# Kernel optimization log

Measured on AMD Instinct MI355X. Metric: run time of the kernel, lower is better.

The kernel has to match this reference:

```python
import jax, jax.numpy as jnp
import numpy as np

IN_CH, OUT_CH, HID, NHEAD = 4, 1, 256, 8
VDIM = HID // NHEAD
LOCALITIES = (2.0, 10.0, 10.0, 10.0, 10.0, 200.0)
N_BLOCKS = len(LOCALITIES) - 2
INPUT_RES, LATENT_RES, OUTPUT_RES = (64, 64), (32, 32), (64, 64)
BATCH = 8


def pairwise_dist(res1x, res1y, res2x, res2y):
    gx1 = jnp.linspace(0, 1, res1x + 1)[:-1]
    gy1 = jnp.linspace(0, 1, res1y + 1)[:-1]
    g1x, g1y = jnp.meshgrid(gx1, gy1, indexing='xy')
    grid1 = jnp.stack([g1x.flatten(), g1y.flatten()], axis=-1)
    gx2 = jnp.linspace(0, 1, res2x + 1)[:-1]
    gy2 = jnp.linspace(0, 1, res2y + 1)[:-1]
    g2x, g2y = jnp.meshgrid(gx2, gy2, indexing='xy')
    grid2 = jnp.stack([g2x.flatten(), g2y.flatten()], axis=-1)
    diff = grid1[:, None, :] - grid2[None, :, :]
    return (jnp.sum(diff ** 2, axis=-1) / 2.0).astype(jnp.float32)


def pos_att(m_dist, x, r, w, locality):
    # m_dist:[Nq,Nk]  x:[B,Nk,HID]  r:[H,1,1]  w:[H,HID,VDIM]
    scale = jnp.tan(0.25 * jnp.pi * (1 - 1e-07) * (1 + jnp.sin(r)))
    sd = m_dist[None, :, :] * scale  # [H,Nq,Nk]
    if locality <= 100:
        thr = jnp.percentile(sd, locality, axis=-1, keepdims=True)
        sd = jnp.where(sd <= thr, sd, jnp.inf)
    att = jax.nn.softmax(-sd, axis=-1)  # [H,Nq,Nk]
    value = jnp.einsum('bnj,hjk->bhnk', x, w)  # [B,H,Nk,VDIM]
    out = jnp.einsum('hjn,bhnk->bhjk', att, value)  # [B,H,Nq,VDIM]
    out = jnp.transpose(out, (0, 2, 1, 3)).reshape(x.shape[0], m_dist.shape[0], -1)
    return jax.nn.gelu(out)


def lin(x, w, b):
    # eqx.nn.Linear: w:[out,in], b:[out]
    return jnp.einsum('bni,oi->bno', x, w) + b


def setup_inputs() -> dict:
    key = jax.random.key(0)
    ks = jax.random.split(key, 20)
    Ni = INPUT_RES[0] * INPUT_RES[1]
    s_h = 1.0 / jnp.sqrt(HID)
    s_in = 1.0 / jnp.sqrt(IN_CH)
    return {
        'x': jax.random.normal(ks[0], (BATCH, Ni, IN_CH), jnp.float32),
        'en_fc1_w': jax.random.uniform(ks[1], (HID, IN_CH), jnp.float32, -s_in, s_in),
        'en_fc1_b': jax.random.uniform(ks[2], (HID,), jnp.float32, -s_in, s_in),
        'down_r': jax.random.normal(ks[3], (NHEAD, 1, 1), jnp.float32),
        'down_w': jax.random.normal(ks[4], (NHEAD, HID, VDIM), jnp.float32) * s_h,
        'pa_r': jax.random.normal(ks[5], (N_BLOCKS, NHEAD, 1, 1), jnp.float32),
        'pa_w': jax.random.normal(ks[6], (N_BLOCKS, NHEAD, HID, VDIM), jnp.float32) * s_h,
        'mlp1_w': jax.random.uniform(ks[7], (N_BLOCKS, HID, HID), jnp.float32, -s_h, s_h),
        'mlp1_b': jax.random.uniform(ks[8], (N_BLOCKS, HID), jnp.float32, -s_h, s_h),
        'mlp2_w': jax.random.uniform(ks[9], (N_BLOCKS, HID, HID), jnp.float32, -s_h, s_h),
        'mlp2_b': jax.random.uniform(ks[10], (N_BLOCKS, HID), jnp.float32, -s_h, s_h),
        'res_w': jax.random.uniform(ks[11], (N_BLOCKS, HID, HID), jnp.float32, -s_h, s_h),
        'res_b': jax.random.uniform(ks[12], (N_BLOCKS, HID), jnp.float32, -s_h, s_h),
        'up_r': jax.random.normal(ks[13], (NHEAD, 1, 1), jnp.float32),
        'up_w': jax.random.normal(ks[14], (NHEAD, HID, VDIM), jnp.float32) * s_h,
        'de_fc1_w': jax.random.uniform(ks[15], (HID, HID), jnp.float32, -s_h, s_h),
        'de_fc1_b': jax.random.uniform(ks[16], (HID,), jnp.float32, -s_h, s_h),
        'de_fc2_w': jax.random.uniform(ks[17], (OUT_CH, HID), jnp.float32, -s_h, s_h),
        'de_fc2_b': jax.random.uniform(ks[18], (OUT_CH,), jnp.float32, -s_h, s_h),
    }


def reference(x, en_fc1_w, en_fc1_b, down_r, down_w, pa_r, pa_w,
              mlp1_w, mlp1_b, mlp2_w, mlp2_b, res_w, res_b,
              up_r, up_w, de_fc1_w, de_fc1_b, de_fc2_w, de_fc2_b):
    m_dist_down = pairwise_dist(LATENT_RES[0], LATENT_RES[1], INPUT_RES[0], INPUT_RES[1])
    m_dist_proc = pairwise_dist(LATENT_RES[0], LATENT_RES[1], LATENT_RES[0], LATENT_RES[1])
    m_dist_up = pairwise_dist(OUTPUT_RES[0], OUTPUT_RES[1], LATENT_RES[0], LATENT_RES[1])

    h = jax.nn.gelu(lin(x, en_fc1_w, en_fc1_b))
    h = pos_att(m_dist_down, h, down_r, down_w, LOCALITIES[0])
    for i in range(N_BLOCKS):
        pa_out = pos_att(m_dist_proc, h, pa_r[i], pa_w[i], LOCALITIES[1 + i])
        mlp_out = lin(jax.nn.gelu(lin(pa_out, mlp1_w[i], mlp1_b[i])), mlp2_w[i], mlp2_b[i])
        residual = lin(h, res_w[i], res_b[i])
        h = jax.nn.gelu(mlp_out + residual)
    h = pos_att(m_dist_up, h, up_r, up_w, LOCALITIES[-1])
    h = jax.nn.gelu(lin(h, de_fc1_w, de_fc1_b))
    return lin(h, de_fc2_w, de_fc2_b)
```

## Files before the change

kernel.cpp:

```cpp
#include <hip/hip_runtime.h>
#include <math.h>


#define PI_F 3.14159265358979323846f

typedef __attribute__((ext_vector_type(8))) short short8;
typedef __attribute__((ext_vector_type(4))) float float4v;
typedef __attribute__((ext_vector_type(4))) unsigned short ushort4v;

__device__ __forceinline__ float gelu_f(float x) {
  float u = 0.7978845608028654f * (x + 0.044715f * x * x * x);
  float e = __expf(2.0f * u);
  float t = 1.0f - 2.0f / (e + 1.0f);
  return 0.5f * x * (1.0f + t);
}

__device__ __forceinline__ float head_scale(float r) {
  return tanf(0.25f * PI_F * (1.0f - 1e-7f) * (1.0f + sinf(r)));
}

__device__ __forceinline__ unsigned short f2bf(float f) {
  union { float f; unsigned u; } c; c.f = f;
  unsigned u = c.u + 0x7FFFu + ((c.u >> 16) & 1u);
  return (unsigned short)(u >> 16);
}
__device__ __forceinline__ float bf2f(unsigned short h) {
  union { unsigned u; float f; } c; c.u = ((unsigned)h) << 16;
  return c.f;
}
__device__ __forceinline__ void split_bf(float f, unsigned short& hi,
                                         unsigned short& lo) {
  hi = f2bf(f);
  lo = f2bf(f - bf2f(hi));
}

__device__ __forceinline__ void gl16(const void* g, void* l) {
  __builtin_amdgcn_global_load_lds(
      (const __attribute__((address_space(1))) unsigned int*)g,
      (__attribute__((address_space(3))) unsigned int*)l, 16, 0, 0);
}

__global__ __launch_bounds__(256) void k_enc(
    const float* __restrict__ x, const float* __restrict__ w,
    const float* __restrict__ b, unsigned short* __restrict__ ahi,
    unsigned short* __restrict__ alo) {
  int row = blockIdx.x;
  int o = threadIdx.x;
  float4 xv = *(const float4*)(x + (size_t)row * 4);
  float4 wv = *(const float4*)(w + (size_t)o * 4);
  float s = xv.x * wv.x + xv.y * wv.y + xv.z * wv.z + xv.w * wv.w + b[o];
  s = gelu_f(s);
  unsigned short hi, lo;
  split_bf(s, hi, lo);
  ahi[(size_t)row * 256 + o] = hi;
  alo[(size_t)row * 256 + o] = lo;
}

__global__ __launch_bounds__(256) void k_split_all(
    const float* __restrict__ down_w, const float* __restrict__ de1_w,
    const float* __restrict__ up_w, const float* __restrict__ pa_w,
    const float* __restrict__ mlp1_w, const float* __restrict__ mlp2_w,
    const float* __restrict__ res_w, unsigned short* __restrict__ whi,
    unsigned short* __restrict__ wlo) {
  int i = blockIdx.x * 256 + threadIdx.x;
  float f;
  if (i < 65536) {
    int n = i >> 8, k = i & 255;
    f = down_w[(n >> 5) * 8192 + k * 32 + (n & 31)];
  } else if (i < 131072) {
    f = de1_w[i - 65536];
  } else if (i < 196608) {
    int j = i - 131072;
    int n = j >> 8, k = j & 255;
    f = up_w[(n >> 5) * 8192 + k * 32 + (n & 31)];
  } else if (i < 458752) {
    int j = i - 196608;
    int blk = j >> 16, r = j & 65535;
    int n = r >> 8, k = r & 255;
    f = pa_w[(size_t)blk * 65536 + (n >> 5) * 8192 + k * 32 + (n & 31)];
  } else if (i < 720896) {
    f = mlp1_w[i - 458752];
  } else if (i < 983040) {
    f = mlp2_w[i - 720896];
  } else {
    f = res_w[i - 983040];
  }
  unsigned short hi, lo;
  split_bf(f, hi, lo);
  whi[i] = hi;
  wlo[i] = lo;
}

template <int KRES, int CXM, int NPT, int TARGET, int TMAX>
__global__ __launch_bounds__(256) void k_thresh(int* __restrict__ thr) {
  __shared__ int wsum[4];
  int q = blockIdx.x, tid = threadIdx.x;
  int qx = q & 31, qy = q >> 5;
  int cx = qx * CXM, cy = qy * CXM;
  int d[NPT];
#pragma unroll
  for (int j = 0; j < NPT; ++j) {
    int k = tid * NPT + j;
    int kx = k & (KRES - 1), ky = k / KRES;
    int dx = cx - kx, dy = cy - ky;
    d[j] = dx * dx + dy * dy;
  }
  int lo = 0, hi = TMAX;
  while (lo < hi) {
    int mid = (lo + hi) >> 1;
    int c = 0;
#pragma unroll
    for (int j = 0; j < NPT; ++j) c += (d[j] <= mid) ? 1 : 0;
#pragma unroll
    for (int off = 32; off > 0; off >>= 1) c += __shfl_down(c, off, 64);
    if ((tid & 63) == 0) wsum[tid >> 6] = c;
    __syncthreads();
    int total = wsum[0] + wsum[1] + wsum[2] + wsum[3];
    __syncthreads();
    if (total >= TARGET) hi = mid; else lo = mid + 1;
  }
  if (tid == 0) thr[q] = lo;
}

template <int KRES, int CXM, int DSHIFT, int J2>
__global__ __launch_bounds__(256) void k_klist2(
    const float* __restrict__ rvec, const int* __restrict__ thr,
    int* __restrict__ klist2, int* __restrict__ kcnt2,
    float* __restrict__ wlist2) {
  __shared__ int cntS;
  __shared__ int sidx[J2];
  __shared__ int sdv[J2][4];
  __shared__ float denS[8][4];
  int tile = blockIdx.x, tid = threadIdx.x;
  int tx = tile & 15, ty = tile >> 4;
  int cxA[4], cyA[4], T[4];
#pragma unroll
  for (int i = 0; i < 4; ++i) {
    int qx = 2 * tx + (i & 1), qy = 2 * ty + (i >> 1);
    cxA[i] = qx * CXM; cyA[i] = qy * CXM;
    T[i] = thr[qy * 32 + qx];
  }
  if (tid == 0) cntS = 0;
  __syncthreads();
  int x0 = KRES - 1, x1 = 0, y0 = KRES - 1, y1 = 0;
#pragma unroll
  for (int i = 0; i < 4; ++i) {
    int rad = (int)sqrtf((float)T[i]);
    while ((rad + 1) * (rad + 1) <= T[i]) ++rad;
    while (rad > 0 && rad * rad > T[i]) --rad;
    x0 = min(x0, max(0, cxA[i] - rad));
    x1 = max(x1, min(KRES - 1, cxA[i] + rad));
    y0 = min(y0, max(0, cyA[i] - rad));
    y1 = max(y1, min(KRES - 1, cyA[i] + rad));
  }
  int W = x1 - x0 + 1, H = y1 - y0 + 1, tot = W * H;
  for (int p = tid; p < tot; p += 256) {
    int kx = x0 + p % W, ky = y0 + p / W;
    int d[4]; bool keep = false;
#pragma unroll
    for (int i = 0; i < 4; ++i) {
      int dx = cxA[i] - kx, dy = cyA[i] - ky;
      d[i] = dx * dx + dy * dy;
      keep = keep || (d[i] <= T[i]);
    }
    if (keep) {
      int s = atomicAdd(&cntS, 1);
      if (s < J2) {
        sidx[s] = ky * KRES + kx;
#pragma unroll
        for (int i = 0; i < 4; ++i) sdv[s][i] = d[i];
      }
    }
  }
  __syncthreads();
  int cnt = min(cntS, J2);
  int h = tid >> 5, lane = tid & 31;
  float sc = head_scale(rvec[h]) * (1.0f / (float)(1 << DSHIFT));
  float den[4] = {0.f, 0.f, 0.f, 0.f};
  for (int j = lane; j < cnt; j += 32) {
#pragma unroll
    for (int i = 0; i < 4; ++i)
      if (sdv[j][i] <= T[i]) den[i] += __expf(-sc * (float)sdv[j][i]);
  }
#pragma unroll
  for (int i = 0; i < 4; ++i) {
    float d0 = den[i];
#pragma unroll
    for (int off = 16; off > 0; off >>= 1) d0 += __shfl_down(d0, off, 32);
    if (lane == 0) denS[h][i] = d0;
  }
  __syncthreads();
  float inv[4];
#pragma unroll
  for (int i = 0; i < 4; ++i) inv[i] = 1.0f / denS[h][i];
  for (int j = lane; j < cnt; j += 32) {
    float w[4];
#pragma unroll
    for (int i = 0; i < 4; ++i)
      w[i] = (sdv[j][i] <= T[i]) ? __expf(-sc * (float)sdv[j][i]) * inv[i] : 0.f;
    float4v wv = {w[0], w[1], w[2], w[3]};
    *(float4v*)&wlist2[(((size_t)h * 256 + tile) * J2 + j) * 4] = wv;
  }
  if (tid == 0) kcnt2[tile] = cnt;
  if (h == 0)
    for (int j = lane; j < cnt; j += 32) klist2[(size_t)tile * J2 + j] = sidx[j];
}

template <int NK, int J2>
__global__ __launch_bounds__(256) void k_att3(
    const float* __restrict__ value,
    const int* __restrict__ klist2, const int* __restrict__ kcnt2,
    const float* __restrict__ wlist2, unsigned short* __restrict__ ohi,
    unsigned short* __restrict__ olo) {
  __shared__ int kls[J2];
  __shared__ float4v wls[J2];
  __shared__ float4v part[4][4][64];
  int blk = blockIdx.x;
  int tile = blk >> 3, h = blk & 7;
  int tid = threadIdx.x, g = tid & 63, s = tid >> 6;
  int cnt = kcnt2[tile];
  for (int j = tid; j < cnt; j += 256) {
    kls[j] = klist2[(size_t)tile * J2 + j];
    wls[j] = *(const float4v*)&wlist2[(((size_t)h * 256 + tile) * J2 + j) * 4];
  }
  __syncthreads();
  const float* vb = value + (size_t)h * NK * 256 + g * 4;
  float4v acc[4];
#pragma unroll
  for (int i = 0; i < 4; ++i) acc[i] = (float4v)0.0f;
  for (int j = s; j < cnt; j += 4) {
    int row = kls[j];
    float4v v = *(const float4v*)(vb + (size_t)row * 256);
    float4v w = wls[j];
    acc[0] += w.x * v;
    acc[1] += w.y * v;
    acc[2] += w.z * v;
    acc[3] += w.w * v;
  }
#pragma unroll
  for (int i = 0; i < 4; ++i) part[s][i][g] = acc[i];
  __syncthreads();
  if (tid < 64) {
    int g2 = tid;
    int ttx = tile & 15, tty = tile >> 4;
    int batch = g2 >> 3, v0 = (g2 & 7) * 4;
#pragma unroll
    for (int i = 0; i < 4; ++i) {
      float4v o4 = part[0][i][g2] + part[1][i][g2] + part[2][i][g2] +
                   part[3][i][g2];
      int q = (2 * tty + (i >> 1)) * 32 + 2 * ttx + (i & 1);
      size_t idx = ((size_t)batch * 1024 + q) * 256 + h * 32 + v0;
      ushort4v hv, lv;
#pragma unroll
      for (int c = 0; c < 4; ++c) {
        float oo = gelu_f(o4[c]);
        unsigned short hi, lo;
        split_bf(oo, hi, lo);
        hv[c] = hi; lv[c] = lo;
      }
      *(ushort4v*)(ohi + idx) = hv;
      *(ushort4v*)(olo + idx) = lv;
    }
  }
}

template <int BM, int BN, bool DUAL, int OL, bool GEL, bool OHILO>
__global__ __launch_bounds__(256) void k_gn(
    const unsigned short* __restrict__ A1hi, const unsigned short* __restrict__ A1lo,
    const unsigned short* __restrict__ W1hi, const unsigned short* __restrict__ W1lo,
    const unsigned short* __restrict__ A2hi, const unsigned short* __restrict__ A2lo,
    const unsigned short* __restrict__ W2hi, const unsigned short* __restrict__ W2lo,
    const float* __restrict__ bias, const float* __restrict__ bias2,
    float* __restrict__ outf, unsigned short* __restrict__ ohi,
    unsigned short* __restrict__ olo, int NS) {
  constexpr int MS = BM / 32;
  constexpr int NF = BN / 32;
  constexpr int NWCH = BN / 32;
  constexpr int NACH = BM / 32;
  __shared__ alignas(16) unsigned short Wh_s[BN * 64];
  __shared__ alignas(16) unsigned short Wl_s[BN * 64];
  __shared__ alignas(16) unsigned short Ah_s[BM * 64];
  __shared__ alignas(16) unsigned short Al_s[BM * 64];
  int tid = threadIdx.x;
  constexpr int BPM = 256 / BN;
  int b = blockIdx.x;
  int m0 = (b / BPM) * BM;
  int n_off = (b % BPM) * BN;
  int w = tid >> 6, lane = tid & 63;
  int quad = lane >> 4, l16 = lane & 15;
  int wm = (w >> 1) * (BM / 2), wn = (w & 1) * (BN / 2);

  int wgo[NWCH], wls_[NWCH];
#pragma unroll
  for (int i = 0; i < NWCH; ++i) {
    int rem = tid + i * 256;
    int r = rem >> 3, s = rem & 7, c = s ^ (r & 7);
    wgo[i] = (n_off + r) * 256 + c * 8;
    wls_[i] = rem * 8;
  }
  int ago[NACH], als_[NACH];
#pragma unroll
  for (int i = 0; i < NACH; ++i) {
    int rem = tid + i * 256;
    int r = rem >> 3, s = rem & 7, c = s ^ (r & 7);
    ago[i] = r * 256 + c * 8;
    als_[i] = rem * 8;
  }

  float4v acc[MS][NF];
#pragma unroll
  for (int i = 0; i < MS; ++i)
#pragma unroll
    for (int n = 0; n < NF; ++n) acc[i][n] = (float4v)0.0f;

  const int NSTEP = DUAL ? 8 : 4;
  for (int st = 0; st < NSTEP; ++st) {
    const unsigned short *pWh, *pWl, *pAh, *pAl;
    if (DUAL && st >= 4) { pWh = W2hi; pWl = W2lo; pAh = A2hi; pAl = A2lo; }
    else { pWh = W1hi; pWl = W1lo; pAh = A1hi; pAl = A1lo; }
    int kb = (st & 3) * 64;
    __syncthreads();
#pragma unroll
    for (int i = 0; i < NWCH; ++i) {
      gl16(pWh + wgo[i] + kb, &Wh_s[wls_[i]]);
      gl16(pWl + wgo[i] + kb, &Wl_s[wls_[i]]);
    }
    size_t ab = (size_t)m0 * 256 + kb;
#pragma unroll
    for (int i = 0; i < NACH; ++i) {
      gl16(pAh + ab + ago[i], &Ah_s[als_[i]]);
      gl16(pAl + ab + ago[i], &Al_s[als_[i]]);
    }
    __syncthreads();
#pragma unroll
    for (int ks2 = 0; ks2 < 2; ++ks2) {
      short8 ah[MS], al[MS];
#pragma unroll
      for (int ms = 0; ms < MS; ++ms) {
        int ra = wm + ms * 16 + l16;
        int c = (ks2 * 4 + quad) ^ (ra & 7);
        ah[ms] = *(const short8*)&Ah_s[ra * 64 + c * 8];
        al[ms] = *(const short8*)&Al_s[ra * 64 + c * 8];
      }
#pragma unroll
      for (int ns = 0; ns < NF; ++ns) {
        int rb = wn + ns * 16 + l16;
        int c = (ks2 * 4 + quad) ^ (rb & 7);
        short8 bh = *(const short8*)&Wh_s[rb * 64 + c * 8];
        short8 bl = *(const short8*)&Wl_s[rb * 64 + c * 8];
#pragma unroll
        for (int ms = 0; ms < MS; ++ms) {
          acc[ms][ns] = __builtin_amdgcn_mfma_f32_16x16x32_bf16(
              ah[ms], bh, acc[ms][ns], 0, 0, 0);
          acc[ms][ns] = __builtin_amdgcn_mfma_f32_16x16x32_bf16(
              ah[ms], bl, acc[ms][ns], 0, 0, 0);
          acc[ms][ns] = __builtin_amdgcn_mfma_f32_16x16x32_bf16(
              al[ms], bh, acc[ms][ns], 0, 0, 0);
        }
      }
    }
  }
#pragma unroll
  for (int ms = 0; ms < MS; ++ms) {
#pragma unroll
    for (int ns = 0; ns < NF; ++ns) {
      int n = n_off + wn + ns * 16 + l16;
      float bv = bias ? bias[n] : 0.0f;
      if (DUAL && bias2) bv += bias2[n];
#pragma unroll
      for (int r = 0; r < 4; ++r) {
        int m = m0 + wm + ms * 16 + quad * 4 + r;
        float c = acc[ms][ns][r] + bv;
        if (GEL) c = gelu_f(c);
        if (OHILO) {
          unsigned short chi, clo;
          split_bf(c, chi, clo);
          ohi[(size_t)m * 256 + n] = chi;
          olo[(size_t)m * 256 + n] = clo;
        } else if (OL == 0) {
          outf[(size_t)m * 256 + n] = c;
        } else {
          int N = 1 << NS;
          int bb = m >> NS, rr = m & (N - 1);
          outf[(((size_t)(n >> 5) * N + rr) * 8 + bb) * 32 + (n & 31)] = c;
        }
      }
    }
  }
}

__global__ __launch_bounds__(256) void k_up_s1(
    const float* __restrict__ value,
    const float* __restrict__ rvec, float* __restrict__ T) {
  __shared__ float AxL[64][33];
  int ky = blockIdx.x, h = blockIdx.y, tid = threadIdx.x;
  float sc = head_scale(rvec[h]) * (1.0f / 8192.0f);
  float v[32];
  const float* vb = value + ((size_t)h * 1024 + ky * 32) * 256 + tid;
#pragma unroll
  for (int kx = 0; kx < 32; ++kx) v[kx] = vb[kx * 256];
  if (tid < 64) {
    int qx = tid, dxmin = qx & 1;
    for (int kx = 0; kx < 32; ++kx) {
      int dx = qx - 2 * kx;
      AxL[qx][kx] = __expf(-sc * (float)(dx * dx - dxmin));
    }
  }
  __syncthreads();
  float* tb = T + (((size_t)h * 64) * 32 + ky) * 256 + tid;
  for (int qx = 0; qx < 64; ++qx) {
    float acc = 0.f;
#pragma unroll
    for (int kx = 0; kx < 32; ++kx) acc += AxL[qx][kx] * v[kx];
    tb[(size_t)qx * 32 * 256] = acc;
  }
}

__global__ __launch_bounds__(256) void k_up_s2(
    const float* __restrict__ T, const float* __restrict__ rvec,
    unsigned short* __restrict__ ohi, unsigned short* __restrict__ olo) {
  __shared__ float AyL[64][33];
  __shared__ float Sy[64];
  __shared__ float SxS;
  int qx = blockIdx.x, h = blockIdx.y, tid = threadIdx.x;
  float sc = head_scale(rvec[h]) * (1.0f / 8192.0f);
  float t[32];
  const float* tb = T + ((size_t)h * 64 + qx) * 32 * 256 + tid;
#pragma unroll
  for (int ky = 0; ky < 32; ++ky) t[ky] = tb[ky * 256];
  if (tid < 64) {
    int qy = tid, dymin = qy & 1;
    float s = 0.f;
    for (int ky = 0; ky < 32; ++ky) {
      int dy = qy - 2 * ky;
      float e = __expf(-sc * (float)(dy * dy - dymin));
      AyL[qy][ky] = e;
      s += e;
    }
    Sy[qy] = s;
  } else if (tid >= 64 && tid < 96) {
    int kx = tid - 64, dxmin = qx & 1;
    int dx = qx - 2 * kx;
    float e = __expf(-sc * (float)(dx * dx - dxmin));
#pragma unroll
    for (int off = 16; off > 0; off >>= 1) e += __shfl_down(e, off, 32);
    if (kx == 0) SxS = e;
  }
  __syncthreads();
  float invSx = 1.0f / SxS;
  int b = tid >> 5, v = tid & 31;
  size_t base = ((size_t)b * 4096 + qx) * 256 + h * 32 + v;
  for (int qy = 0; qy < 64; ++qy) {
    float acc = 0.f;
#pragma unroll
    for (int ky = 0; ky < 32; ++ky) acc += AyL[qy][ky] * t[ky];
    float o = gelu_f(acc * invSx / Sy[qy]);
    unsigned short hi, lo;
    split_bf(o, hi, lo);
    size_t idx = base + (size_t)qy * 64 * 256;
    ohi[idx] = hi;
    olo[idx] = lo;
  }
}

__global__ __launch_bounds__(256) void k_fc2(const float* __restrict__ h,
                                             const float* __restrict__ w,
                                             const float* __restrict__ b,
                                             float* __restrict__ out) {
  int row = blockIdx.x * 4 + (threadIdx.x >> 6);
  int lane = threadIdx.x & 63;
  float4 hv = *(const float4*)(h + (size_t)row * 256 + lane * 4);
  float4 wv = *(const float4*)(w + lane * 4);
  float s = hv.x * wv.x + hv.y * wv.y + hv.z * wv.z + hv.w * wv.w;
#pragma unroll
  for (int off = 32; off > 0; off >>= 1) s += __shfl_down(s, off, 64);
  if (lane == 0) out[row] = s + b[0];
}

extern "C" void kernel_launch(void* const* d_in, const int* in_sizes, int n_in,
                              void* d_out, int out_size, void* d_ws,
                              size_t ws_size, hipStream_t stream) {
  const float* x      = (const float*)d_in[0];
  const float* en_w   = (const float*)d_in[1];
  const float* en_b   = (const float*)d_in[2];
  const float* down_r = (const float*)d_in[3];
  const float* down_w = (const float*)d_in[4];
  const float* pa_r   = (const float*)d_in[5];
  const float* pa_w   = (const float*)d_in[6];
  const float* mlp1_w = (const float*)d_in[7];
  const float* mlp1_b = (const float*)d_in[8];
  const float* mlp2_w = (const float*)d_in[9];
  const float* mlp2_b = (const float*)d_in[10];
  const float* res_w  = (const float*)d_in[11];
  const float* res_b  = (const float*)d_in[12];
  const float* up_r   = (const float*)d_in[13];
  const float* up_w   = (const float*)d_in[14];
  const float* de1_w  = (const float*)d_in[15];
  const float* de1_b  = (const float*)d_in[16];
  const float* de2_w  = (const float*)d_in[17];
  const float* de2_b  = (const float*)d_in[18];
  float* out = (float*)d_out;

  constexpr int J2 = 256;
  float* ws = (float*)d_ws;
  unsigned short* Ahi = (unsigned short*)ws;
  unsigned short* Alo = Ahi + 8388608;
  float* B = ws + 8388608;
  float* Tbuf = B + 2097152;
  unsigned short* hAhi = (unsigned short*)(ws + 16777216);
  unsigned short* hAlo = hAhi + 2097152;
  unsigned short* hBhi = hAlo + 2097152;
  unsigned short* hBlo = hBhi + 2097152;
  unsigned short* pahi = hBlo + 2097152;
  unsigned short* palo = pahi + 2097152;
  unsigned short* m1hi = palo + 2097152;
  unsigned short* m1lo = m1hi + 2097152;
  int* thrD = (int*)(ws + 25165824);
  int* thrP = thrD + 1024;
  int* cntD2 = thrP + 1024;
  int* cntP2 = cntD2 + 256;
  int* klD2 = cntP2 + 256;
  int* klP2 = klD2 + 256 * J2;
  float* wlD2 = (float*)(klP2 + 256 * J2);
  float* wlP2 = wlD2 + 2097152;
  unsigned short* Whi = (unsigned short*)(wlP2 + 2097152);
  unsigned short* Wlo = Whi + 1245184;
  const int WO_DOWN = 0, WO_DE1 = 65536, WO_UP = 131072, WO_PA = 196608,
            WO_MLP1 = 458752, WO_MLP2 = 720896, WO_RES = 983040;

  k_enc<<<32768, 256, 0, stream>>>(x, en_w, en_b, Ahi, Alo);
  k_split_all<<<4864, 256, 0, stream>>>(down_w, de1_w, up_w, pa_w, mlp1_w,
                                        mlp2_w, res_w, Whi, Wlo);
  k_thresh<64, 2, 16, 82, 7938><<<1024, 256, 0, stream>>>(thrD);
  k_thresh<32, 1, 4, 103, 1922><<<1024, 256, 0, stream>>>(thrP);
  k_klist2<64, 2, 13, J2><<<256, 256, 0, stream>>>(down_r, thrD, klD2, cntD2,
                                                   wlD2);
  k_klist2<32, 1, 11, J2><<<256, 256, 0, stream>>>(pa_r, thrP, klP2, cntP2,
                                                   wlP2);
  k_gn<64, 256, false, 1, false, false><<<512, 256, 0, stream>>>(
      Ahi, Alo, Whi + WO_DOWN, Wlo + WO_DOWN, nullptr, nullptr, nullptr,
      nullptr, nullptr, nullptr, B, nullptr, nullptr, 12);
  k_att3<4096, J2><<<2048, 256, 0, stream>>>(B, klD2, cntD2, wlD2, hAhi, hAlo);
  for (int i = 0; i < 4; ++i) {
    const unsigned short* hih = (i & 1) ? hBhi : hAhi;
    const unsigned short* hil = (i & 1) ? hBlo : hAlo;
    unsigned short* hoh = (i & 1) ? hAhi : hBhi;
    unsigned short* hol = (i & 1) ? hAlo : hBlo;
    k_gn<32, 128, false, 1, false, false><<<512, 256, 0, stream>>>(
        hih, hil, Whi + WO_PA + i * 65536, Wlo + WO_PA + i * 65536, nullptr,
        nullptr, nullptr, nullptr, nullptr, nullptr, B, nullptr, nullptr, 10);
    k_att3<1024, J2><<<2048, 256, 0, stream>>>(B, klP2, cntP2, wlP2, pahi,
                                               palo);
    k_gn<32, 128, false, 0, true, true><<<512, 256, 0, stream>>>(
        pahi, palo, Whi + WO_MLP1 + i * 65536, Wlo + WO_MLP1 + i * 65536,
        nullptr, nullptr, nullptr, nullptr, mlp1_b + i * 256, nullptr, nullptr,
        m1hi, m1lo, 0);
    k_gn<32, 128, true, 0, true, true><<<512, 256, 0, stream>>>(
        m1hi, m1lo, Whi + WO_MLP2 + i * 65536, Wlo + WO_MLP2 + i * 65536, hih,
        hil, Whi + WO_RES + i * 65536, Wlo + WO_RES + i * 65536,
        mlp2_b + i * 256, res_b + i * 256, nullptr, hoh, hol, 0);
  }
  k_gn<32, 128, false, 1, false, false><<<512, 256, 0, stream>>>(
      hAhi, hAlo, Whi + WO_UP, Wlo + WO_UP, nullptr, nullptr, nullptr, nullptr,
      nullptr, nullptr, B, nullptr, nullptr, 10);
  k_up_s1<<<dim3(32, 8), 256, 0, stream>>>(B, up_r, Tbuf);
  k_up_s2<<<dim3(64, 8), 256, 0, stream>>>(Tbuf, up_r, Ahi, Alo);
  k_gn<64, 256, false, 0, true, false><<<512, 256, 0, stream>>>(
      Ahi, Alo, Whi + WO_DE1, Wlo + WO_DE1, nullptr, nullptr, nullptr, nullptr,
      de1_b, nullptr, B, nullptr, nullptr, 0);
  k_fc2<<<8192, 256, 0, stream>>>(B, de2_w, de2_b, out);
}
```

Measured before the change: 450.3 us.

## Double-buffer GEMM LDS tiles, swizzle block order, vectorize encoder stores

The hi/lo split-bf16 GEMM kernel now keeps two LDS buffers and issues the async global-to-LDS loads for the next K step before computing the current one. This removes one barrier per step and overlaps memory with MFMA work, at the cost of doubling LDS use, which may lower occupancy for the 64x256 tile. Block indices for multi-N-block launches are remapped so that neighbouring blocks share M tiles. The encoder kernel now has each thread compute four outputs and write them with vector stores, which cuts the grid by four.

```diff
diff --git a/kernel.cpp b/kernel.cpp
--- a/kernel.cpp
+++ b/kernel.cpp
@@ -44,16 +44,22 @@
     const float* __restrict__ x, const float* __restrict__ w,
     const float* __restrict__ b, unsigned short* __restrict__ ahi,
     unsigned short* __restrict__ alo) {
-  int row = blockIdx.x;
-  int o = threadIdx.x;
+  int row = blockIdx.x * 4 + (threadIdx.x >> 6);
+  int o = (threadIdx.x & 63) * 4;
   float4 xv = *(const float4*)(x + (size_t)row * 4);
-  float4 wv = *(const float4*)(w + (size_t)o * 4);
-  float s = xv.x * wv.x + xv.y * wv.y + xv.z * wv.z + xv.w * wv.w + b[o];
-  s = gelu_f(s);
-  unsigned short hi, lo;
-  split_bf(s, hi, lo);
-  ahi[(size_t)row * 256 + o] = hi;
-  alo[(size_t)row * 256 + o] = lo;
+  ushort4v hv, lv;
+#pragma unroll
+  for (int i = 0; i < 4; ++i) {
+    float4 wv = *(const float4*)(w + (size_t)(o + i) * 4);
+    float s = xv.x * wv.x + xv.y * wv.y + xv.z * wv.z + xv.w * wv.w + b[o + i];
+    s = gelu_f(s);
+    unsigned short hi, lo;
+    split_bf(s, hi, lo);
+    hv[i] = hi; lv[i] = lo;
+  }
+  size_t idx = (size_t)row * 256 + o;
+  *(ushort4v*)(ahi + idx) = hv;
+  *(ushort4v*)(alo + idx) = lv;
 }
 
 __global__ __launch_bounds__(256) void k_split_all(
@@ -277,15 +283,21 @@
   constexpr int NF = BN / 32;
   constexpr int NWCH = BN / 32;
   constexpr int NACH = BM / 32;
-  __shared__ alignas(16) unsigned short Wh_s[BN * 64];
-  __shared__ alignas(16) unsigned short Wl_s[BN * 64];
-  __shared__ alignas(16) unsigned short Ah_s[BM * 64];
-  __shared__ alignas(16) unsigned short Al_s[BM * 64];
+  __shared__ alignas(16) unsigned short Wh_s[2][BN * 64];
+  __shared__ alignas(16) unsigned short Wl_s[2][BN * 64];
+  __shared__ alignas(16) unsigned short Ah_s[2][BM * 64];
+  __shared__ alignas(16) unsigned short Al_s[2][BM * 64];
   int tid = threadIdx.x;
   constexpr int BPM = 256 / BN;
   int b = blockIdx.x;
-  int m0 = (b / BPM) * BM;
-  int n_off = (b % BPM) * BN;
+  int m0, n_off;
+  if (BPM == 1) {
+    m0 = b * BM; n_off = 0;
+  } else {
+    int x = b & 7, t = b >> 3;
+    int nh = t & 1, mt = (t >> 1) * 8 + x;
+    m0 = mt * BM; n_off = nh * BN;
+  }
   int w = tid >> 6, lane = tid & 63;
   int quad = lane >> 4, l16 = lane & 15;
   int wm = (w >> 1) * (BM / 2), wn = (w & 1) * (BN / 2);
@@ -314,24 +326,30 @@
     for (int n = 0; n < NF; ++n) acc[i][n] = (float4v)0.0f;
 
   const int NSTEP = DUAL ? 8 : 4;
-  for (int st = 0; st < NSTEP; ++st) {
+
+  auto STAGE = [&](int st, int buf) {
     const unsigned short *pWh, *pWl, *pAh, *pAl;
     if (DUAL && st >= 4) { pWh = W2hi; pWl = W2lo; pAh = A2hi; pAl = A2lo; }
     else { pWh = W1hi; pWl = W1lo; pAh = A1hi; pAl = A1lo; }
     int kb = (st & 3) * 64;
-    __syncthreads();
 #pragma unroll
     for (int i = 0; i < NWCH; ++i) {
-      gl16(pWh + wgo[i] + kb, &Wh_s[wls_[i]]);
-      gl16(pWl + wgo[i] + kb, &Wl_s[wls_[i]]);
+      gl16(pWh + wgo[i] + kb, &Wh_s[buf][wls_[i]]);
+      gl16(pWl + wgo[i] + kb, &Wl_s[buf][wls_[i]]);
     }
     size_t ab = (size_t)m0 * 256 + kb;
 #pragma unroll
     for (int i = 0; i < NACH; ++i) {
-      gl16(pAh + ab + ago[i], &Ah_s[als_[i]]);
-      gl16(pAl + ab + ago[i], &Al_s[als_[i]]);
-    }
-    __syncthreads();
+      gl16(pAh + ab + ago[i], &Ah_s[buf][als_[i]]);
+      gl16(pAl + ab + ago[i], &Al_s[buf][als_[i]]);
+    }
+  };
+
+  STAGE(0, 0);
+  __syncthreads();
+  for (int st = 0; st < NSTEP; ++st) {
+    int cur = st & 1;
+    if (st + 1 < NSTEP) STAGE(st + 1, cur ^ 1);
 #pragma unroll
     for (int ks2 = 0; ks2 < 2; ++ks2) {
       short8 ah[MS], al[MS];
@@ -339,15 +357,15 @@
       for (int ms = 0; ms < MS; ++ms) {
         int ra = wm + ms * 16 + l16;
         int c = (ks2 * 4 + quad) ^ (ra & 7);
-        ah[ms] = *(const short8*)&Ah_s[ra * 64 + c * 8];
-        al[ms] = *(const short8*)&Al_s[ra * 64 + c * 8];
+        ah[ms] = *(const short8*)&Ah_s[cur][ra * 64 + c * 8];
+        al[ms] = *(const short8*)&Al_s[cur][ra * 64 + c * 8];
       }
 #pragma unroll
       for (int ns = 0; ns < NF; ++ns) {
         int rb = wn + ns * 16 + l16;
         int c = (ks2 * 4 + quad) ^ (rb & 7);
-        short8 bh = *(const short8*)&Wh_s[rb * 64 + c * 8];
-        short8 bl = *(const short8*)&Wl_s[rb * 64 + c * 8];
+        short8 bh = *(const short8*)&Wh_s[cur][rb * 64 + c * 8];
+        short8 bl = *(const short8*)&Wl_s[cur][rb * 64 + c * 8];
 #pragma unroll
         for (int ms = 0; ms < MS; ++ms) {
           acc[ms][ns] = __builtin_amdgcn_mfma_f32_16x16x32_bf16(
@@ -359,6 +377,7 @@
         }
       }
     }
+    __syncthreads();
   }
 #pragma unroll
   for (int ms = 0; ms < MS; ++ms) {
@@ -528,7 +547,7 @@
   const int WO_DOWN = 0, WO_DE1 = 65536, WO_UP = 131072, WO_PA = 196608,
             WO_MLP1 = 458752, WO_MLP2 = 720896, WO_RES = 983040;
 
-  k_enc<<<32768, 256, 0, stream>>>(x, en_w, en_b, Ahi, Alo);
+  k_enc<<<8192, 256, 0, stream>>>(x, en_w, en_b, Ahi, Alo);
   k_split_all<<<4864, 256, 0, stream>>>(down_w, de1_w, up_w, pa_w, mlp1_w,
                                         mlp2_w, res_w, Whi, Wlo);
   k_thresh<64, 2, 16, 82, 7938><<<1024, 256, 0, stream>>>(thrD);
```

Result: slower. 546.1 us (+21.3%).
